# Kernel tuning notes

Measured on AMD Instinct MI355X. Metric: run time of the kernel, lower is better.

Reference implementation:

```python
import jax, jax.numpy as jnp
import numpy as np
from functools import partial

N = 10  # n_qubits (static)


def _rx(state, w, theta, n):
    # state: [B, 2^n] complex64; RX(theta) on wire w (wire 0 = most significant)
    B = state.shape[0]
    st = state.reshape(B, 2 ** w, 2, 2 ** (n - 1 - w))
    half = jnp.asarray(theta, state.real.dtype) * 0.5
    c = jnp.cos(half).reshape(-1, 1, 1)
    s = jnp.sin(half).reshape(-1, 1, 1)
    s0, s1 = st[:, :, 0], st[:, :, 1]
    n0 = c * s0 - 1j * s * s1
    n1 = -1j * s * s0 + c * s1
    return jnp.stack([n0, n1], axis=2).reshape(B, 2 ** n)


def _cnot(state, control, target, n):
    B = state.shape[0]
    a, bb = (control, target) if control < target else (target, control)
    st = state.reshape(B, 2 ** a, 2, 2 ** (bb - a - 1), 2, 2 ** (n - 1 - bb))
    if control == a:
        # control is axis 2, target axis 4: flip target where control==1
        c1 = jnp.flip(st[:, :, 1], axis=3)
        st = jnp.stack([st[:, :, 0], c1], axis=2)
    else:
        # control is axis 4, target axis 2: flip axis-2 slice where control==1
        c1 = jnp.flip(st[:, :, :, :, 1], axis=1)
        st = jnp.stack([st[:, :, :, :, 0], c1], axis=4)
    return st.reshape(B, 2 ** n)


def _expect_z(state, n):
    B = state.shape[0]
    probs = jnp.abs(state) ** 2  # [B, 2^n]
    es = []
    for w in range(n):
        p = probs.reshape(B, 2 ** w, 2, 2 ** (n - 1 - w))
        es.append(p[:, :, 0].sum((1, 2)) - p[:, :, 1].sum((1, 2)))
    return jnp.stack(es, axis=1)  # [B, n]


def _qlayer(x, theta, n):
    # x: [B, n] encoder angles; theta: [n] trainable RX angles
    B = x.shape[0]
    state = jnp.zeros((B, 2 ** n), jnp.complex64).at[:, 0].set(1.0)
    for w in range(n):
        state = _rx(state, w, x[:, w], n)
    for w in range(n):
        state = _rx(state, w, theta[w], n)
    for w in range(n - 1):
        state = _cnot(state, w, w + 1, n)
    state = _cnot(state, n - 1, 0, n)
    return _expect_z(state, n)


def setup_inputs() -> dict:
    key = jax.random.key(0)
    k1, k2, k3, k4 = jax.random.split(key, 4)
    T, B, D, H = 64, 256, 246, N
    inputs = jax.random.normal(k1, (T, B, D), jnp.float32)
    fan_in = D + H
    W = jax.random.normal(k2, (4, N, fan_in), jnp.float32) / np.sqrt(fan_in)
    b = jax.random.normal(k3, (4, N), jnp.float32) * 0.01
    thetas = jax.random.normal(k4, (4, N), jnp.float32)
    return {"inputs": inputs, "W": W, "b": b, "thetas": thetas}


def reference(inputs, W, b, thetas):
    T, B, D = inputs.shape
    H = thetas.shape[-1]
    qlayer4 = jax.vmap(partial(_qlayer, n=N))  # over the 4 gates

    def step(carry, x_t):
        hx, cx = carry
        comb = jnp.concatenate([x_t, hx], axis=1)          # [B, D+H]
        z = jnp.einsum('bi,goi->gbo', comb, W) + b[:, None, :]  # [4, B, n]
        gates = qlayer4(z, thetas)                          # [4, B, n]
        f = jax.nn.sigmoid(gates[0])
        i = jax.nn.sigmoid(gates[1])
        g = jnp.tanh(gates[2])
        o = jax.nn.sigmoid(gates[3])
        cx = f * cx + i * g
        hx = o * jnp.tanh(cx)
        return (hx, cx), hx

    hx0 = jnp.zeros((B, H), inputs.dtype)
    cx0 = jnp.zeros((B, H), inputs.dtype)
    (hx, cx), outputs = jax.lax.scan(step, (hx0, cx0), inputs)
    return outputs, hx, cx
```

## Files before the change

### kernel.cpp

```cpp
#include <hip/hip_runtime.h>
#include <hip/hip_bf16.h>

#define D_IN   246
#define NW     10
#define NG     4
#define NOUT   40
#define FANIN  256
#define BATCH  256
#define TSTEPS 64
#define WP_ELEMS (NG * D_IN * 16)

__global__ __launch_bounds__(256) void k_wt(const float* __restrict__ W,
                                            float* __restrict__ Wp) {
    int e = blockIdx.x * 256 + threadIdx.x;
    if (e >= WP_ELEMS) return;
    int o = e & 15;
    int i = (e >> 4) % D_IN;
    int g = e / (16 * D_IN);
    float v = (o < NW) ? W[(g * NW + o) * FANIN + i] : 0.f;
    Wp[e] = v;
}

__global__ __launch_bounds__(512) void k_zx(
    const float* __restrict__ x,
    const float* __restrict__ Wp,
    const float* __restrict__ bias,
    const float* __restrict__ theta,
    float* __restrict__ zxT)
{
    const int t    = blockIdx.x;
    const int bq   = blockIdx.y;
    const int tid  = threadIdx.x;
    const int lane = tid & 63;
    const int wv   = __builtin_amdgcn_readfirstlane(tid >> 6);
    const int g    = wv & 3;
    const int kh   = wv >> 2;

    __shared__ float xl[64 * D_IN];
    __shared__ float pr[NG][64][NW];

    const float* xsrc = x + ((size_t)t * BATCH + bq * 64) * D_IN;
    for (int k = tid; k < 64 * 123; k += 512) {
        int row = k / 123;
        int j   = k - row * 123;
        float2 v = *reinterpret_cast<const float2*>(xsrc + row * D_IN + 2 * j);
        *reinterpret_cast<float2*>(xl + row * D_IN + 2 * j) = v;
    }
    __syncthreads();

    const int khbase = kh ? 124 : 0;
    const int npairs = kh ? 61 : 62;

    float acc[NW];
#pragma unroll
    for (int o = 0; o < NW; ++o) acc[o] = 0.f;

    const float* wg = Wp + (g * D_IN + khbase) * 16;
    const float* xr = xl + lane * D_IN + khbase;

#pragma unroll 2
    for (int ii = 0; ii < npairs; ++ii) {
        float2 xv = *reinterpret_cast<const float2*>(xr + 2 * ii);
#pragma unroll
        for (int o = 0; o < NW; ++o) {
            acc[o] += xv.x * wg[(2 * ii)     * 16 + o];
            acc[o] += xv.y * wg[(2 * ii + 1) * 16 + o];
        }
    }

    if (kh == 1) {
#pragma unroll
        for (int o = 0; o < NW; ++o) pr[g][lane][o] = acc[o];
    }
    __syncthreads();

    if (kh == 0) {
#pragma unroll
        for (int o = 0; o < NW; ++o)
            acc[o] += pr[g][lane][o] + bias[g * NW + o] + theta[g * NW + o];
        const int b = bq * 64 + lane;
        float* zo = zxT + ((size_t)b * TSTEPS + t) * NOUT + g * NW;
#pragma unroll
        for (int q = 0; q < 5; ++q)
            *reinterpret_cast<float2*>(zo + 2 * q) = make_float2(acc[2 * q], acc[2 * q + 1]);
    }
}

template <int CTRL>
__device__ __forceinline__ float dpp_shr_mul(float p) {
    int up = __builtin_amdgcn_update_dpp(__float_as_int(1.0f), __float_as_int(p),
                                         CTRL, 0xF, 0xF, false);
    return p * __int_as_float(up);
}

__global__ __launch_bounds__(64) void k_scan(
    const float* __restrict__ zxT,
    const float* __restrict__ W,
    float* __restrict__ out,
    float* __restrict__ hxout,
    float* __restrict__ cxout)
{
    const int b    = blockIdx.x;
    const int lane = threadIdx.x;
    const int r    = lane >> 4;
    const int o    = lane & 15;
    const bool act = (o < NW);
    const int oc   = act ? o : 0;

    __shared__ float zl[TSTEPS * NOUT];

    {
        const float4* src4 = reinterpret_cast<const float4*>(zxT + (size_t)b * TSTEPS * NOUT);
        float4* dst4 = reinterpret_cast<float4*>(zl);
#pragma unroll
        for (int q = 0; q < 10; ++q) dst4[q * 64 + lane] = src4[q * 64 + lane];
    }

    float wh[NW];
#pragma unroll
    for (int j = 0; j < NW; ++j)
        wh[j] = W[(r * NW + oc) * FANIN + D_IN + j];

    const float am = (r == 2) ? 2.f : 1.f;
    const float vm = (r == 2) ? 2.f : 1.f;
    const float vc = (r == 2) ? -1.f : 0.f;
    const int idx1 = (lane ^ 16) << 2;
    const int idx2 = (lane ^ 32) << 2;
    const int idx3 = (lane ^ 48) << 2;
    const bool q1 = (r & 1) != 0;
    const bool q2 = (r & 2) != 0;

    __syncthreads();

    float hx_s[NW];
#pragma unroll
    for (int j = 0; j < NW; ++j) hx_s[j] = 0.f;

    float cx = 0.f, hv = 0.f;
    const int cidx = r * NW + oc;
    float zc = act ? zl[cidx] : 0.f;

    for (int t = 0; t < TSTEPS; ++t) {
        float zn = zl[(((t + 1) & 63) * NOUT) + cidx];

        float s0 = zc, s1 = 0.f;
#pragma unroll
        for (int j = 0; j < 5; ++j) {
            s0 = fmaf(hx_s[2 * j],     wh[2 * j],     s0);
            s1 = fmaf(hx_s[2 * j + 1], wh[2 * j + 1], s1);
        }
        float z = s0 + s1;

        float cv = __cosf(z);

        float p = cv;
        p = dpp_shr_mul<0x111>(p);
        p = dpp_shr_mul<0x112>(p);
        p = dpp_shr_mul<0x114>(p);
        p = dpp_shr_mul<0x118>(p);

        float e  = __expf(-(p * am));
        float sg = __fdividef(1.f, 1.f + e);
        float val = fmaf(sg, vm, vc);

        int vi = __float_as_int(val);
        float a1 = __int_as_float(__builtin_amdgcn_ds_bpermute(idx1, vi));
        float a2 = __int_as_float(__builtin_amdgcn_ds_bpermute(idx2, vi));
        float a3 = __int_as_float(__builtin_amdgcn_ds_bpermute(idx3, vi));

        float fv = q2 ? (q1 ? a3 : a2) : (q1 ? a1 : val);
        float iv = q2 ? (q1 ? a2 : a3) : (q1 ? val : a1);
        float gv = q2 ? (q1 ? a1 : val) : (q1 ? a3 : a2);
        float ov = q2 ? (q1 ? val : a1) : (q1 ? a2 : a3);

        cx = fmaf(fv, cx, iv * gv);
        float e2 = __expf(cx + cx);
        float th = 1.f - __fdividef(2.f, 1.f + e2);
        hv = ov * th;

        if (r == 0 && act) out[((size_t)t * BATCH + b) * NW + o] = hv;

#pragma unroll
        for (int j = 0; j < NW; ++j)
            hx_s[j] = __int_as_float(__builtin_amdgcn_readlane(__float_as_int(hv), j));

        zc = zn;
    }

    if (r == 0 && act) {
        hxout[b * NW + o] = hv;
        cxout[b * NW + o] = cx;
    }
}

extern "C" void kernel_launch(void* const* d_in, const int* in_sizes, int n_in,
                              void* d_out, int out_size, void* d_ws, size_t ws_size,
                              hipStream_t stream) {
    const float* x     = (const float*)d_in[0];
    const float* W     = (const float*)d_in[1];
    const float* bias  = (const float*)d_in[2];
    const float* theta = (const float*)d_in[3];

    float* out   = (float*)d_out;
    float* hxout = out + (size_t)TSTEPS * BATCH * NW;
    float* cxout = hxout + (size_t)BATCH * NW;

    float* Wp  = (float*)d_ws;
    float* zxT = Wp + WP_ELEMS;

    k_wt<<<(WP_ELEMS + 255) / 256, 256, 0, stream>>>(W, Wp);
    dim3 g1(TSTEPS, 4);
    k_zx<<<g1, 512, 0, stream>>>(x, Wp, bias, theta, zxT);
    k_scan<<<BATCH, 64, 0, stream>>>(zxT, W, out, hxout, cxout);
}
```

Before: 103.0 us.

## Fuse input projection into scan kernel, one block per batch row

The separate input-projection kernel and the recurrent scan kernel are merged into one kernel with one 256-thread block per batch element. Each block loads all 64 timesteps of its x row into LDS, and four waves (one per gate) compute the projections straight into a padded LDS buffer. Wave 0 then runs the recurrent scan. This removes one launch and the global zxT round trip, at the cost of a strided x gather per block and three waves sitting idle during the serial scan.

```diff
diff --git a/kernel.cpp b/kernel.cpp
--- a/kernel.cpp
+++ b/kernel.cpp
@@ -4,10 +4,10 @@
 #define D_IN   246
 #define NW     10
 #define NG     4
-#define NOUT   40
 #define FANIN  256
 #define BATCH  256
 #define TSTEPS 64
+#define ZSTR   42
 #define WP_ELEMS (NG * D_IN * 16)
 
 __global__ __launch_bounds__(256) void k_wt(const float* __restrict__ W,
@@ -21,71 +21,6 @@
     Wp[e] = v;
 }
 
-__global__ __launch_bounds__(512) void k_zx(
-    const float* __restrict__ x,
-    const float* __restrict__ Wp,
-    const float* __restrict__ bias,
-    const float* __restrict__ theta,
-    float* __restrict__ zxT)
-{
-    const int t    = blockIdx.x;
-    const int bq   = blockIdx.y;
-    const int tid  = threadIdx.x;
-    const int lane = tid & 63;
-    const int wv   = __builtin_amdgcn_readfirstlane(tid >> 6);
-    const int g    = wv & 3;
-    const int kh   = wv >> 2;
-
-    __shared__ float xl[64 * D_IN];
-    __shared__ float pr[NG][64][NW];
-
-    const float* xsrc = x + ((size_t)t * BATCH + bq * 64) * D_IN;
-    for (int k = tid; k < 64 * 123; k += 512) {
-        int row = k / 123;
-        int j   = k - row * 123;
-        float2 v = *reinterpret_cast<const float2*>(xsrc + row * D_IN + 2 * j);
-        *reinterpret_cast<float2*>(xl + row * D_IN + 2 * j) = v;
-    }
-    __syncthreads();
-
-    const int khbase = kh ? 124 : 0;
-    const int npairs = kh ? 61 : 62;
-
-    float acc[NW];
-#pragma unroll
-    for (int o = 0; o < NW; ++o) acc[o] = 0.f;
-
-    const float* wg = Wp + (g * D_IN + khbase) * 16;
-    const float* xr = xl + lane * D_IN + khbase;
-
-#pragma unroll 2
-    for (int ii = 0; ii < npairs; ++ii) {
-        float2 xv = *reinterpret_cast<const float2*>(xr + 2 * ii);
-#pragma unroll
-        for (int o = 0; o < NW; ++o) {
-            acc[o] += xv.x * wg[(2 * ii)     * 16 + o];
-            acc[o] += xv.y * wg[(2 * ii + 1) * 16 + o];
-        }
-    }
-
-    if (kh == 1) {
-#pragma unroll
-        for (int o = 0; o < NW; ++o) pr[g][lane][o] = acc[o];
-    }
-    __syncthreads();
-
-    if (kh == 0) {
-#pragma unroll
-        for (int o = 0; o < NW; ++o)
-            acc[o] += pr[g][lane][o] + bias[g * NW + o] + theta[g * NW + o];
-        const int b = bq * 64 + lane;
-        float* zo = zxT + ((size_t)b * TSTEPS + t) * NOUT + g * NW;
-#pragma unroll
-        for (int q = 0; q < 5; ++q)
-            *reinterpret_cast<float2*>(zo + 2 * q) = make_float2(acc[2 * q], acc[2 * q + 1]);
-    }
-}
-
 template <int CTRL>
 __device__ __forceinline__ float dpp_shr_mul(float p) {
     int up = __builtin_amdgcn_update_dpp(__float_as_int(1.0f), __float_as_int(p),
@@ -93,28 +28,68 @@
     return p * __int_as_float(up);
 }
 
-__global__ __launch_bounds__(64) void k_scan(
-    const float* __restrict__ zxT,
+__global__ __launch_bounds__(256) void k_fused(
+    const float* __restrict__ x,
+    const float* __restrict__ Wp,
+    const float* __restrict__ bias,
+    const float* __restrict__ theta,
     const float* __restrict__ W,
     float* __restrict__ out,
     float* __restrict__ hxout,
     float* __restrict__ cxout)
 {
     const int b    = blockIdx.x;
-    const int lane = threadIdx.x;
-    const int r    = lane >> 4;
-    const int o    = lane & 15;
-    const bool act = (o < NW);
-    const int oc   = act ? o : 0;
+    const int tid  = threadIdx.x;
+    const int lane = tid & 63;
+    const int wv   = __builtin_amdgcn_readfirstlane(tid >> 6);
 
-    __shared__ float zl[TSTEPS * NOUT];
+    __shared__ float xl[64 * D_IN];
+    __shared__ float zl[TSTEPS * ZSTR];
+
+    for (int row = wv; row < 64; row += 4) {
+        const float* src = x + ((size_t)row * BATCH + b) * D_IN;
+        float* dst = xl + row * D_IN;
+        for (int j = lane; j < 123; j += 64) {
+            float2 v = *reinterpret_cast<const float2*>(src + 2 * j);
+            *reinterpret_cast<float2*>(dst + 2 * j) = v;
+        }
+    }
+    __syncthreads();
 
     {
-        const float4* src4 = reinterpret_cast<const float4*>(zxT + (size_t)b * TSTEPS * NOUT);
-        float4* dst4 = reinterpret_cast<float4*>(zl);
+        const int g = wv;
+        float acc[NW];
 #pragma unroll
-        for (int q = 0; q < 10; ++q) dst4[q * 64 + lane] = src4[q * 64 + lane];
+        for (int o = 0; o < NW; ++o)
+            acc[o] = bias[g * NW + o] + theta[g * NW + o];
+
+        const float* wg = Wp + g * D_IN * 16;
+        const float* xr = xl + lane * D_IN;
+
+#pragma unroll 4
+        for (int ii = 0; ii < 123; ++ii) {
+            float2 xv = *reinterpret_cast<const float2*>(xr + 2 * ii);
+#pragma unroll
+            for (int o = 0; o < NW; ++o) {
+                acc[o] = fmaf(xv.x, wg[(2 * ii) * 16 + o], acc[o]);
+                acc[o] = fmaf(xv.y, wg[(2 * ii + 1) * 16 + o], acc[o]);
+            }
+        }
+
+        float* zo = zl + lane * ZSTR + g * NW;
+#pragma unroll
+        for (int q = 0; q < 5; ++q)
+            *reinterpret_cast<float2*>(zo + 2 * q) = make_float2(acc[2 * q], acc[2 * q + 1]);
     }
+    __syncthreads();
+
+    if (wv != 0) return;
+
+    const int r   = lane >> 4;
+    const int o   = lane & 15;
+    const bool act = (o < NW);
+    const int oc  = act ? o : 0;
+    const int cidx = r * NW + oc;
 
     float wh[NW];
 #pragma unroll
@@ -130,18 +105,15 @@
     const bool q1 = (r & 1) != 0;
     const bool q2 = (r & 2) != 0;
 
-    __syncthreads();
-
     float hx_s[NW];
 #pragma unroll
     for (int j = 0; j < NW; ++j) hx_s[j] = 0.f;
 
     float cx = 0.f, hv = 0.f;
-    const int cidx = r * NW + oc;
-    float zc = act ? zl[cidx] : 0.f;
+    float zc = zl[cidx];
 
     for (int t = 0; t < TSTEPS; ++t) {
-        float zn = zl[(((t + 1) & 63) * NOUT) + cidx];
+        float zn = zl[((t + 1) & 63) * ZSTR + cidx];
 
         float s0 = zc, s1 = 0.f;
 #pragma unroll
@@ -205,11 +177,8 @@
     float* hxout = out + (size_t)TSTEPS * BATCH * NW;
     float* cxout = hxout + (size_t)BATCH * NW;
 
-    float* Wp  = (float*)d_ws;
-    float* zxT = Wp + WP_ELEMS;
+    float* Wp = (float*)d_ws;
 
     k_wt<<<(WP_ELEMS + 255) / 256, 256, 0, stream>>>(W, Wp);
-    dim3 g1(TSTEPS, 4);
-    k_zx<<<g1, 512, 0, stream>>>(x, Wp, bias, theta, zxT);
-    k_scan<<<BATCH, 64, 0, stream>>>(zxT, W, out, hxout, cxout);
+    k_fused<<<BATCH, 256, 0, stream>>>(x, Wp, bias, theta, W, out, hxout, cxout);
 }
```

Result: slower. 121.8 us (+18.3%).

## Drop weight-transpose kernel, stage weights in LDS, pack scan waves per block

Applied to the files above, without the earlier changes.

Removes the separate weight-repacking kernel launch. Each GEMM block now loads W directly into an LDS layout interleaved by input pair, so the inner loop reads five float4s per pair instead of scattered scalars. The scan kernel packs eight batch rows per 512-thread block and streams z values straight from global memory rather than staging them in LDS, cutting the block count and the LDS copy. The trade-off is that every GEMM block redundantly loads all of W, and the scan's global z loads sit on the serial recurrence path.

```diff
diff --git a/kernel.cpp b/kernel.cpp
--- a/kernel.cpp
+++ b/kernel.cpp
@@ -8,22 +8,12 @@
 #define FANIN  256
 #define BATCH  256
 #define TSTEPS 64
-#define WP_ELEMS (NG * D_IN * 16)
-
-__global__ __launch_bounds__(256) void k_wt(const float* __restrict__ W,
-                                            float* __restrict__ Wp) {
-    int e = blockIdx.x * 256 + threadIdx.x;
-    if (e >= WP_ELEMS) return;
-    int o = e & 15;
-    int i = (e >> 4) % D_IN;
-    int g = e / (16 * D_IN);
-    float v = (o < NW) ? W[(g * NW + o) * FANIN + i] : 0.f;
-    Wp[e] = v;
-}
-
-__global__ __launch_bounds__(512) void k_zx(
+#define NPAIR  123
+#define WL_ELEMS (NG * NPAIR * 20)
+
+__global__ __launch_bounds__(512) void k_gemm(
     const float* __restrict__ x,
-    const float* __restrict__ Wp,
+    const float* __restrict__ W,
     const float* __restrict__ bias,
     const float* __restrict__ theta,
     float* __restrict__ zxT)
@@ -37,35 +27,50 @@
     const int kh   = wv >> 2;
 
     __shared__ float xl[64 * D_IN];
+    __shared__ float Wl[WL_ELEMS];
     __shared__ float pr[NG][64][NW];
 
+    for (int e = tid; e < WL_ELEMS; e += 512) {
+        int q = e % 20;
+        int j = (e / 20) % NPAIR;
+        int gg = e / (20 * NPAIR);
+        int o = q >> 1, k = q & 1;
+        Wl[e] = W[(gg * NW + o) * FANIN + (2 * j + k)];
+    }
     const float* xsrc = x + ((size_t)t * BATCH + bq * 64) * D_IN;
-    for (int k = tid; k < 64 * 123; k += 512) {
-        int row = k / 123;
-        int j   = k - row * 123;
+    for (int k = tid; k < 64 * NPAIR; k += 512) {
+        int row = k / NPAIR;
+        int j   = k - row * NPAIR;
         float2 v = *reinterpret_cast<const float2*>(xsrc + row * D_IN + 2 * j);
         *reinterpret_cast<float2*>(xl + row * D_IN + 2 * j) = v;
     }
     __syncthreads();
 
-    const int khbase = kh ? 124 : 0;
+    const int jstart = kh ? 62 : 0;
     const int npairs = kh ? 61 : 62;
 
     float acc[NW];
 #pragma unroll
     for (int o = 0; o < NW; ++o) acc[o] = 0.f;
 
-    const float* wg = Wp + (g * D_IN + khbase) * 16;
-    const float* xr = xl + lane * D_IN + khbase;
+    const float* wg = Wl + (g * NPAIR + jstart) * 20;
+    const float* xr = xl + lane * D_IN + 2 * jstart;
 
 #pragma unroll 2
-    for (int ii = 0; ii < npairs; ++ii) {
-        float2 xv = *reinterpret_cast<const float2*>(xr + 2 * ii);
-#pragma unroll
-        for (int o = 0; o < NW; ++o) {
-            acc[o] += xv.x * wg[(2 * ii)     * 16 + o];
-            acc[o] += xv.y * wg[(2 * ii + 1) * 16 + o];
-        }
+    for (int jj = 0; jj < npairs; ++jj) {
+        float2 xv = *reinterpret_cast<const float2*>(xr + 2 * jj);
+        const float4* w4 = reinterpret_cast<const float4*>(wg + jj * 20);
+        float4 wa0 = w4[0], wb = w4[1], wc = w4[2], wd = w4[3], we = w4[4];
+        acc[0] = fmaf(xv.x, wa0.x, fmaf(xv.y, wa0.y, acc[0]));
+        acc[1] = fmaf(xv.x, wa0.z, fmaf(xv.y, wa0.w, acc[1]));
+        acc[2] = fmaf(xv.x, wb.x,  fmaf(xv.y, wb.y,  acc[2]));
+        acc[3] = fmaf(xv.x, wb.z,  fmaf(xv.y, wb.w,  acc[3]));
+        acc[4] = fmaf(xv.x, wc.x,  fmaf(xv.y, wc.y,  acc[4]));
+        acc[5] = fmaf(xv.x, wc.z,  fmaf(xv.y, wc.w,  acc[5]));
+        acc[6] = fmaf(xv.x, wd.x,  fmaf(xv.y, wd.y,  acc[6]));
+        acc[7] = fmaf(xv.x, wd.z,  fmaf(xv.y, wd.w,  acc[7]));
+        acc[8] = fmaf(xv.x, we.x,  fmaf(xv.y, we.y,  acc[8]));
+        acc[9] = fmaf(xv.x, we.z,  fmaf(xv.y, we.w,  acc[9]));
     }
 
     if (kh == 1) {
@@ -75,14 +80,14 @@
     __syncthreads();
 
     if (kh == 0) {
-#pragma unroll
-        for (int o = 0; o < NW; ++o)
-            acc[o] += pr[g][lane][o] + bias[g * NW + o] + theta[g * NW + o];
         const int b = bq * 64 + lane;
         float* zo = zxT + ((size_t)b * TSTEPS + t) * NOUT + g * NW;
 #pragma unroll
-        for (int q = 0; q < 5; ++q)
-            *reinterpret_cast<float2*>(zo + 2 * q) = make_float2(acc[2 * q], acc[2 * q + 1]);
+        for (int q = 0; q < 5; ++q) {
+            float v0 = acc[2*q]   + pr[g][lane][2*q]   + bias[g*NW + 2*q]   + theta[g*NW + 2*q];
+            float v1 = acc[2*q+1] + pr[g][lane][2*q+1] + bias[g*NW + 2*q+1] + theta[g*NW + 2*q+1];
+            *reinterpret_cast<float2*>(zo + 2 * q) = make_float2(v0, v1);
+        }
     }
 }
 
@@ -93,28 +98,20 @@
     return p * __int_as_float(up);
 }
 
-__global__ __launch_bounds__(64) void k_scan(
+__global__ __launch_bounds__(512) void k_scan(
     const float* __restrict__ zxT,
     const float* __restrict__ W,
     float* __restrict__ out,
     float* __restrict__ hxout,
     float* __restrict__ cxout)
 {
-    const int b    = blockIdx.x;
-    const int lane = threadIdx.x;
+    const int wv   = __builtin_amdgcn_readfirstlane(threadIdx.x >> 6);
+    const int b    = blockIdx.x * 8 + wv;
+    const int lane = threadIdx.x & 63;
     const int r    = lane >> 4;
     const int o    = lane & 15;
     const bool act = (o < NW);
     const int oc   = act ? o : 0;
-
-    __shared__ float zl[TSTEPS * NOUT];
-
-    {
-        const float4* src4 = reinterpret_cast<const float4*>(zxT + (size_t)b * TSTEPS * NOUT);
-        float4* dst4 = reinterpret_cast<float4*>(zl);
-#pragma unroll
-        for (int q = 0; q < 10; ++q) dst4[q * 64 + lane] = src4[q * 64 + lane];
-    }
 
     float wh[NW];
 #pragma unroll
@@ -130,18 +127,17 @@
     const bool q1 = (r & 1) != 0;
     const bool q2 = (r & 2) != 0;
 
-    __syncthreads();
-
     float hx_s[NW];
 #pragma unroll
     for (int j = 0; j < NW; ++j) hx_s[j] = 0.f;
-
     float cx = 0.f, hv = 0.f;
-    const int cidx = r * NW + oc;
-    float zc = act ? zl[cidx] : 0.f;
+
+    const float* zp = zxT + (size_t)b * TSTEPS * NOUT + r * NW + oc;
+    float zc = zp[0];
+    float* outp = out + (size_t)b * NW + oc;
 
     for (int t = 0; t < TSTEPS; ++t) {
-        float zn = zl[(((t + 1) & 63) * NOUT) + cidx];
+        float zn = zp[(t + 1) * NOUT];
 
         float s0 = zc, s1 = 0.f;
 #pragma unroll
@@ -178,7 +174,7 @@
         float th = 1.f - __fdividef(2.f, 1.f + e2);
         hv = ov * th;
 
-        if (r == 0 && act) out[((size_t)t * BATCH + b) * NW + o] = hv;
+        if (r == 0 && act) outp[(size_t)t * (BATCH * NW)] = hv;
 
 #pragma unroll
         for (int j = 0; j < NW; ++j)
@@ -205,11 +201,9 @@
     float* hxout = out + (size_t)TSTEPS * BATCH * NW;
     float* cxout = hxout + (size_t)BATCH * NW;
 
-    float* Wp  = (float*)d_ws;
-    float* zxT = Wp + WP_ELEMS;
-
-    k_wt<<<(WP_ELEMS + 255) / 256, 256, 0, stream>>>(W, Wp);
+    float* zxT = (float*)d_ws;
+
     dim3 g1(TSTEPS, 4);
-    k_zx<<<g1, 512, 0, stream>>>(x, Wp, bias, theta, zxT);
-    k_scan<<<BATCH, 64, 0, stream>>>(zxT, W, out, hxout, cxout);
-}
+    k_gemm<<<g1, 512, 0, stream>>>(x, W, bias, theta, zxT);
+    k_scan<<<BATCH / 8, 512, 0, stream>>>(zxT, W, out, hxout, cxout);
+}
```

Measured after the change: 110.0 us. +6.9%, slower.
